# Performance work log

Measured on AMD Instinct MI355X. Metric: run time of the kernel, lower is better.

## Reference

```python
import jax, jax.numpy as jnp
import numpy as np

IMAGE_W = 640
IMAGE_H = 640
ALPHA = 0.25
GAMMA = 2.0
BETA = 1.0 / 9.0
EPS = 1e-4


def _make_anchors(image_w, image_h):
    # standard RetinaNet anchors: 3 ratios x 3 scales per location, 5 FPN levels
    strides = [8, 16, 32, 64, 128]
    base_sizes = [32, 64, 128, 256, 512]
    ratios = np.array([0.5, 1.0, 2.0])
    scales = np.array([2.0 ** 0, 2.0 ** (1.0 / 3.0), 2.0 ** (2.0 / 3.0)])
    all_boxes = []
    for s, b in zip(strides, base_sizes):
        fw, fh = image_w // s, image_h // s
        ws, hs = [], []
        for r in ratios:
            for sc in scales:
                area = (b * sc) ** 2
                w = np.sqrt(area / r)
                ws.append(w)
                hs.append(w * r)
        wh = np.stack([np.array(ws), np.array(hs)], axis=-1).reshape(1, -1, 2)
        cx = (np.arange(fw) + 0.5) * s
        cy = (np.arange(fh) + 0.5) * s
        cx, cy = np.meshgrid(cx, cy)
        ctr = np.stack([cx, cy], axis=-1).reshape(-1, 1, 2)
        boxes = np.concatenate([ctr - 0.5 * wh, ctr + 0.5 * wh], axis=-1).reshape(-1, 4)
        all_boxes.append(boxes)
    return np.concatenate(all_boxes, axis=0).astype(np.float32)  # [76725, 4]


def setup_inputs() -> dict:
    key = jax.random.key(0)
    k1, k2, k3, k4, k5 = jax.random.split(key, 5)
    B, C, M = 4, 80, 16
    anchors = jnp.asarray(_make_anchors(IMAGE_W, IMAGE_H))  # [N,4]
    N = anchors.shape[0]
    batch_anchors = jnp.broadcast_to(anchors[None], (B, N, 4))
    cls_heads = jax.random.uniform(k1, (B, N, C), minval=0.01, maxval=0.99, dtype=jnp.float32)
    reg_heads = jax.random.normal(k2, (B, N, 4), dtype=jnp.float32)
    xy = jax.random.uniform(k3, (B, M, 2), minval=0.0, maxval=480.0)
    wh = jax.random.uniform(k4, (B, M, 2), minval=32.0, maxval=160.0)
    boxes = jnp.concatenate([xy, jnp.minimum(xy + wh, 639.0)], axis=-1)
    labels = jax.random.randint(k5, (B, M), 0, C).astype(jnp.float32)
    valid = jnp.arange(M)[None, :] < 12  # last 4 gt slots are -1 padding
    annotations = jnp.where(valid[..., None],
                            jnp.concatenate([boxes, labels[..., None]], axis=-1),
                            -1.0)
    return {"cls_heads": cls_heads, "reg_heads": reg_heads,
            "batch_anchors": batch_anchors, "annotations": annotations}


def _assign_one_image(anchors, annots):
    # anchors [N,4], annots [M,5] (label<0 == padding)
    valid_gt = annots[:, 4] >= 0.0                                  # [M]
    boxes, cls = annots[:, :4], annots[:, 4]
    area_a = (anchors[:, 2] - anchors[:, 0]) * (anchors[:, 3] - anchors[:, 1])
    area_g = (boxes[:, 2] - boxes[:, 0]) * (boxes[:, 3] - boxes[:, 1])
    lt = jnp.maximum(anchors[:, None, :2], boxes[None, :, :2])      # [N,M,2]
    rb = jnp.minimum(anchors[:, None, 2:], boxes[None, :, 2:])
    wh = jnp.clip(rb - lt, 0.0)
    inter = wh[..., 0] * wh[..., 1]                                 # [N,M]
    iou = inter / (area_a[:, None] + area_g[None, :] - inter)
    iou = jnp.where(valid_gt[None, :], iou, -1.0)                   # ignore padded gts
    idx = jnp.argmax(iou, axis=1)                                   # [N]
    overlap = jnp.max(iou, axis=1)
    gt_box = boxes[idx]                                             # [N,4]
    gt_cls = cls[idx]
    # encode gt box as (tx,ty,tw,th) wrt anchor
    a_wh = anchors[:, 2:] - anchors[:, :2]
    a_ctr = anchors[:, :2] + 0.5 * a_wh
    g_wh = jnp.clip(gt_box[:, 2:] - gt_box[:, :2], 1.0)
    g_ctr = gt_box[:, :2] + 0.5 * g_wh
    targets = jnp.concatenate([(g_ctr - a_ctr) / a_wh, jnp.log(g_wh / a_wh)], axis=1)
    targets = targets / jnp.array([0.1, 0.1, 0.2, 0.2], dtype=targets.dtype)
    label = jnp.full_like(overlap, -1.0)
    label = jnp.where(overlap < 0.4, 0.0, label)
    label = jnp.where(overlap > 0.5, gt_cls + 1.0, label)
    label = jnp.where(jnp.any(valid_gt), label, -1.0)               # no gt -> all ignore
    return targets, label


def reference(cls_heads, reg_heads, batch_anchors, annotations):
    # mask (instead of filter) out-of-border anchors: equivalent to dropping them
    a = batch_anchors
    inside = (a[..., 0] > 0) & (a[..., 1] > 0) & (a[..., 2] < IMAGE_W) & (a[..., 3] < IMAGE_H)
    targets, labels = jax.vmap(_assign_one_image)(batch_anchors, annotations)  # [B,N,4],[B,N]
    labels = jnp.where(inside, labels, -1.0)

    cls_mask = labels >= 0.0          # anchors counted in focal loss
    pos_mask = labels > 0.0           # positive anchors
    pos = jnp.sum(pos_mask, axis=1).astype(cls_heads.dtype)  # [B]

    # focal (cls) loss
    p = jnp.clip(cls_heads, EPS, 1.0 - EPS)                   # [B,N,C]
    num_classes = cls_heads.shape[-1]
    gt_onehot = jax.nn.one_hot(labels.astype(jnp.int32), num_classes + 1,
                               dtype=cls_heads.dtype)[..., 1:]  # [B,N,C]
    is_pos = gt_onehot > 0.5
    alpha_f = jnp.where(is_pos, ALPHA, 1.0 - ALPHA)
    pt = jnp.where(is_pos, p, 1.0 - p)
    focal_w = alpha_f * (1.0 - pt) ** GAMMA
    bce = -gt_onehot * jnp.log(p) - (1.0 - gt_onehot) * jnp.log(1.0 - p)
    fl = focal_w * bce
    cls_per_img = jnp.sum(fl * cls_mask[..., None], axis=(1, 2)) / jnp.maximum(pos, 1.0)

    # smooth-L1 (reg) loss over positive anchors
    x = jnp.abs(reg_heads - targets)
    sl1 = jnp.where(x < BETA, 0.5 * x * x / BETA, x - 0.5 * BETA)
    reg_per_img = jnp.sum(sl1 * pos_mask[..., None], axis=(1, 2)) / jnp.maximum(4.0 * pos, 1.0)

    valid_img = pos > 0.0
    n_valid = jnp.maximum(jnp.sum(valid_img.astype(cls_heads.dtype)), 1.0)
    cls_loss = jnp.sum(jnp.where(valid_img, cls_per_img, 0.0)) / n_valid
    reg_loss = jnp.sum(jnp.where(valid_img, reg_per_img, 0.0)) / n_valid
    return (cls_loss, reg_loss)
```

## Files before the change

### kernel.cpp

```cpp
#include <hip/hip_runtime.h>
#include <cmath>

#define GT_CAP 64

typedef float fvec4 __attribute__((ext_vector_type(4)));

__global__ __launch_bounds__(256) void retina_main(
    const float* __restrict__ cls_heads,
    const float* __restrict__ reg_heads,
    const float* __restrict__ anchors,
    const float* __restrict__ annots,
    float* __restrict__ ws,
    int N, int M, int B)
{
    const int b  = blockIdx.y;
    const int n0 = blockIdx.x << 6;
    const int t  = threadIdx.x;

    __shared__ float s_ann[5 * GT_CAP];
    __shared__ float s_lab[64];
    __shared__ float s_red[12];

    const int mm = (M > GT_CAP) ? GT_CAP : M;
    for (int i = t; i < 5 * mm; i += 256)
        s_ann[i] = annots[(size_t)b * 5 * M + i];
    __syncthreads();

    float reg_acc = 0.0f;
    float pos_cnt = 0.0f;
    float label   = -1.0f;
    if (t < 64) {
        const int n = n0 + t;
        if (n < N) {
            const float4 a = *(const float4*)(anchors + (size_t)n * 4);
            const bool inside = (a.x > 0.0f) && (a.y > 0.0f) &&
                                (a.z < 640.0f) && (a.w < 640.0f);
            if (inside) {
                const float area_a = (a.z - a.x) * (a.w - a.y);
                float best = -3.0e38f;
                int   bi   = 0;
                bool  any  = false;
                for (int m = 0; m < mm; ++m) {
                    const float gx1 = s_ann[m*5+0], gy1 = s_ann[m*5+1];
                    const float gx2 = s_ann[m*5+2], gy2 = s_ann[m*5+3];
                    const float gc  = s_ann[m*5+4];
                    float v = -1.0f;
                    if (gc >= 0.0f) {
                        any = true;
                        const float iw = fmaxf(fminf(a.z, gx2) - fmaxf(a.x, gx1), 0.0f);
                        const float ih = fmaxf(fminf(a.w, gy2) - fmaxf(a.y, gy1), 0.0f);
                        const float inter = iw * ih;
                        v = inter / (area_a + (gx2 - gx1) * (gy2 - gy1) - inter);
                    }
                    if (v > best) { best = v; bi = m; }
                }
                if (any) {
                    if (best < 0.4f)      label = 0.0f;
                    else if (best > 0.5f) label = s_ann[bi*5+4] + 1.0f;
                }
                if (label > 0.0f) {
                    pos_cnt = 1.0f;
                    const float aw = a.z - a.x, ah = a.w - a.y;
                    const float acx = a.x + 0.5f * aw, acy = a.y + 0.5f * ah;
                    const float gw = fmaxf(s_ann[bi*5+2] - s_ann[bi*5+0], 1.0f);
                    const float gh = fmaxf(s_ann[bi*5+3] - s_ann[bi*5+1], 1.0f);
                    const float gcx = s_ann[bi*5+0] + 0.5f * gw;
                    const float gcy = s_ann[bi*5+1] + 0.5f * gh;
                    const float tx = (gcx - acx) / aw * 10.0f;
                    const float ty = (gcy - acy) / ah * 10.0f;
                    const float tw = __logf(gw / aw) * 5.0f;
                    const float th = __logf(gh / ah) * 5.0f;
                    const float4 r = *(const float4*)(reg_heads + ((size_t)b * N + n) * 4);
                    const float dx[4] = { fabsf(r.x - tx), fabsf(r.y - ty),
                                          fabsf(r.z - tw), fabsf(r.w - th) };
                    #pragma unroll
                    for (int j = 0; j < 4; ++j) {
                        const float x = dx[j];
                        reg_acc += (x < (1.0f / 9.0f)) ? 4.5f * x * x
                                                       : x - (1.0f / 18.0f);
                    }
                }
            }
        }
        s_lab[t] = label;
    }
    const int anyValid = __syncthreads_or((t < 64 && label >= 0.0f) ? 1 : 0);

    float cls_acc = 0.0f;
    if (anyValid) {
        const float* cls_base = cls_heads + ((size_t)b * N + n0) * 80;
        float labb[5];
        fvec4 pb[5];
        #pragma unroll
        for (int k = 0; k < 5; ++k) {
            const int e = t + (k << 8);
            const int a = e / 20;
            const float lab = s_lab[a];
            fvec4 v = {0.5f, 0.5f, 0.5f, 0.5f};
            if (lab >= 0.0f)
                v = *(const fvec4*)(cls_base + 4 * e);
            labb[k] = lab; pb[k] = v;
        }
        #pragma unroll
        for (int k = 0; k < 5; ++k) {
            const int e  = t + (k << 8);
            const int c4 = e - (e / 20) * 20;
            const float lab  = labb[k];
            const fvec4 v    = pb[k];
            const float mask = (lab >= 0.0f) ? 1.0f : 0.0f;
            const float pv[4] = { v.x, v.y, v.z, v.w };
            const float cb = (float)(c4 * 4 + 1);
            float local = 0.0f;
            #pragma unroll
            for (int j = 0; j < 4; ++j) {
                const float p = fminf(fmaxf(pv[j], 1.0e-4f), 1.0f - 1.0e-4f);
                const bool  is_pos = (lab == cb + (float)j);
                const float pt     = is_pos ? p : 1.0f - p;
                const float alpha  = is_pos ? 0.25f : 0.75f;
                const float om     = 1.0f - pt;
                local += alpha * om * om * (-__logf(pt));
            }
            cls_acc += mask * local;
        }
    }

    const int lane = t & 63, wid = t >> 6;
    #pragma unroll
    for (int off = 32; off > 0; off >>= 1) {
        cls_acc += __shfl_down(cls_acc, off, 64);
        reg_acc += __shfl_down(reg_acc, off, 64);
        pos_cnt += __shfl_down(pos_cnt, off, 64);
    }
    if (lane == 0) {
        s_red[wid]     = cls_acc;
        s_red[4 + wid] = reg_acc;
        s_red[8 + wid] = pos_cnt;
    }
    __syncthreads();
    if (t == 0) {
        const float c = s_red[0] + s_red[1] + s_red[2]  + s_red[3];
        const float r = s_red[4] + s_red[5] + s_red[6]  + s_red[7];
        const float p = s_red[8] + s_red[9] + s_red[10] + s_red[11];
        if (c != 0.0f) atomicAdd(&ws[b], c);
        if (r != 0.0f) atomicAdd(&ws[B + b], r);
        if (p != 0.0f) atomicAdd(&ws[2 * B + b], p);
    }
}

__global__ void retina_final(const float* __restrict__ ws,
                             float* __restrict__ out, int B)
{
    if (threadIdx.x == 0 && blockIdx.x == 0) {
        float cl = 0.0f, rl = 0.0f, nv = 0.0f;
        for (int b = 0; b < B; ++b) {
            const float pos = ws[2 * B + b];
            if (pos > 0.0f) {
                cl += ws[b]     / fmaxf(pos, 1.0f);
                rl += ws[B + b] / fmaxf(4.0f * pos, 1.0f);
                nv += 1.0f;
            }
        }
        const float n = fmaxf(nv, 1.0f);
        out[0] = cl / n;
        out[1] = rl / n;
    }
}

extern "C" void kernel_launch(void* const* d_in, const int* in_sizes, int n_in,
                              void* d_out, int out_size, void* d_ws, size_t ws_size,
                              hipStream_t stream) {
    const float* cls = (const float*)d_in[0];
    const float* reg = (const float*)d_in[1];
    const float* anc = (const float*)d_in[2];
    const float* ann = (const float*)d_in[3];

    const int B = 4;
    const int N = in_sizes[1] / (4 * B);
    const int M = in_sizes[3] / (5 * B);
    float* ws = (float*)d_ws;

    (void)hipMemsetAsync(d_ws, 0, 12 * sizeof(float), stream);

    dim3 grid((N + 63) / 64, B);
    retina_main<<<grid, 256, 0, stream>>>(cls, reg, anc, ann, ws, N, M, B);
    retina_final<<<1, 64, 0, stream>>>(ws, (float*)d_out, B);
}
```

Measured before the change: 199.2 us.

## Prefetch class tile into LDS asynchronously while computing anchor assignment

Each block now covers 128 anchors, up from 64, and issues global_load_lds async copies of the whole 128x80 class tile into shared memory before the IoU assignment runs. The cls load thus overlaps the anchor/GT matching instead of starting after the label barrier. The annotation staging in shared memory is dropped in favor of direct global reads. The change always loads cls data, even for ignored anchors, and uses about 40KB of LDS per block, which may reduce occupancy. Bandwidth is also wasted on tiles whose anchors are all outside the image.

Result: faster. 175.7 us (-11.8%).

```diff
diff --git a/kernel.cpp b/kernel.cpp
--- a/kernel.cpp
+++ b/kernel.cpp
@@ -1,9 +1,15 @@
 #include <hip/hip_runtime.h>
 #include <cmath>
 
-#define GT_CAP 64
 
 typedef float fvec4 __attribute__((ext_vector_type(4)));
+
+__device__ __forceinline__ void async_ld16(const float* g, float* l) {
+    __builtin_amdgcn_global_load_lds(
+        (const __attribute__((address_space(1))) unsigned int*)g,
+        (__attribute__((address_space(3))) unsigned int*)l,
+        16, 0, 0);
+}
 
 __global__ __launch_bounds__(256) void retina_main(
     const float* __restrict__ cls_heads,
@@ -14,36 +20,42 @@
     int N, int M, int B)
 {
     const int b  = blockIdx.y;
-    const int n0 = blockIdx.x << 6;
+    const int n0 = blockIdx.x << 7;
     const int t  = threadIdx.x;
 
-    __shared__ float s_ann[5 * GT_CAP];
-    __shared__ float s_lab[64];
+    __shared__ float s_cls[128 * 80];
+    __shared__ float s_lab[128];
     __shared__ float s_red[12];
 
-    const int mm = (M > GT_CAP) ? GT_CAP : M;
-    for (int i = t; i < 5 * mm; i += 256)
-        s_ann[i] = annots[(size_t)b * 5 * M + i];
-    __syncthreads();
+    const int tile   = (N - n0 < 128) ? (N - n0) : 128;
+    const int valid4 = tile * 20;
+    const float* gbase = cls_heads + ((size_t)b * N + n0) * 80;
+    #pragma unroll
+    for (int k = 0; k < 10; ++k) {
+        const int idx  = (k << 8) + t;
+        const int gidx = (idx < valid4) ? idx : 0;
+        async_ld16(gbase + 4 * gidx, &s_cls[4 * idx]);
+    }
 
     float reg_acc = 0.0f;
     float pos_cnt = 0.0f;
     float label   = -1.0f;
-    if (t < 64) {
+    if (t < 128) {
         const int n = n0 + t;
         if (n < N) {
             const float4 a = *(const float4*)(anchors + (size_t)n * 4);
             const bool inside = (a.x > 0.0f) && (a.y > 0.0f) &&
                                 (a.z < 640.0f) && (a.w < 640.0f);
             if (inside) {
+                const float* ann = annots + (size_t)b * 5 * M;
                 const float area_a = (a.z - a.x) * (a.w - a.y);
                 float best = -3.0e38f;
                 int   bi   = 0;
                 bool  any  = false;
-                for (int m = 0; m < mm; ++m) {
-                    const float gx1 = s_ann[m*5+0], gy1 = s_ann[m*5+1];
-                    const float gx2 = s_ann[m*5+2], gy2 = s_ann[m*5+3];
-                    const float gc  = s_ann[m*5+4];
+                for (int m = 0; m < M; ++m) {
+                    const float gx1 = ann[m*5+0], gy1 = ann[m*5+1];
+                    const float gx2 = ann[m*5+2], gy2 = ann[m*5+3];
+                    const float gc  = ann[m*5+4];
                     float v = -1.0f;
                     if (gc >= 0.0f) {
                         any = true;
@@ -56,16 +68,16 @@
                 }
                 if (any) {
                     if (best < 0.4f)      label = 0.0f;
-                    else if (best > 0.5f) label = s_ann[bi*5+4] + 1.0f;
+                    else if (best > 0.5f) label = ann[bi*5+4] + 1.0f;
                 }
                 if (label > 0.0f) {
                     pos_cnt = 1.0f;
                     const float aw = a.z - a.x, ah = a.w - a.y;
                     const float acx = a.x + 0.5f * aw, acy = a.y + 0.5f * ah;
-                    const float gw = fmaxf(s_ann[bi*5+2] - s_ann[bi*5+0], 1.0f);
-                    const float gh = fmaxf(s_ann[bi*5+3] - s_ann[bi*5+1], 1.0f);
-                    const float gcx = s_ann[bi*5+0] + 0.5f * gw;
-                    const float gcy = s_ann[bi*5+1] + 0.5f * gh;
+                    const float gw = fmaxf(ann[bi*5+2] - ann[bi*5+0], 1.0f);
+                    const float gh = fmaxf(ann[bi*5+3] - ann[bi*5+1], 1.0f);
+                    const float gcx = ann[bi*5+0] + 0.5f * gw;
+                    const float gcy = ann[bi*5+1] + 0.5f * gh;
                     const float tx = (gcx - acx) / aw * 10.0f;
                     const float ty = (gcy - acy) / ah * 10.0f;
                     const float tw = __logf(gw / aw) * 5.0f;
@@ -84,43 +96,34 @@
         }
         s_lab[t] = label;
     }
-    const int anyValid = __syncthreads_or((t < 64 && label >= 0.0f) ? 1 : 0);
+
+    __builtin_amdgcn_s_waitcnt(0);
+    const int anyValid = __syncthreads_or(label >= 0.0f ? 1 : 0);
 
     float cls_acc = 0.0f;
     if (anyValid) {
-        const float* cls_base = cls_heads + ((size_t)b * N + n0) * 80;
-        float labb[5];
-        fvec4 pb[5];
         #pragma unroll
-        for (int k = 0; k < 5; ++k) {
-            const int e = t + (k << 8);
-            const int a = e / 20;
+        for (int k = 0; k < 10; ++k) {
+            const int e  = (k << 8) + t;
+            const int a  = e / 20;
+            const int c4 = e - a * 20;
             const float lab = s_lab[a];
-            fvec4 v = {0.5f, 0.5f, 0.5f, 0.5f};
-            if (lab >= 0.0f)
-                v = *(const fvec4*)(cls_base + 4 * e);
-            labb[k] = lab; pb[k] = v;
-        }
-        #pragma unroll
-        for (int k = 0; k < 5; ++k) {
-            const int e  = t + (k << 8);
-            const int c4 = e - (e / 20) * 20;
-            const float lab  = labb[k];
-            const fvec4 v    = pb[k];
-            const float mask = (lab >= 0.0f) ? 1.0f : 0.0f;
-            const float pv[4] = { v.x, v.y, v.z, v.w };
-            const float cb = (float)(c4 * 4 + 1);
-            float local = 0.0f;
-            #pragma unroll
-            for (int j = 0; j < 4; ++j) {
-                const float p = fminf(fmaxf(pv[j], 1.0e-4f), 1.0f - 1.0e-4f);
-                const bool  is_pos = (lab == cb + (float)j);
-                const float pt     = is_pos ? p : 1.0f - p;
-                const float alpha  = is_pos ? 0.25f : 0.75f;
-                const float om     = 1.0f - pt;
-                local += alpha * om * om * (-__logf(pt));
+            if (lab >= 0.0f) {
+                const fvec4 v = *(const fvec4*)&s_cls[4 * e];
+                const float pv[4] = { v.x, v.y, v.z, v.w };
+                const float cb = (float)(c4 * 4 + 1);
+                float local = 0.0f;
+                #pragma unroll
+                for (int j = 0; j < 4; ++j) {
+                    const float p = fminf(fmaxf(pv[j], 1.0e-4f), 1.0f - 1.0e-4f);
+                    const bool  is_pos = (lab == cb + (float)j);
+                    const float pt     = is_pos ? p : 1.0f - p;
+                    const float alpha  = is_pos ? 0.25f : 0.75f;
+                    const float om     = 1.0f - pt;
+                    local += alpha * om * om * (-__logf(pt));
+                }
+                cls_acc += local;
             }
-            cls_acc += mask * local;
         }
     }
 
@@ -181,7 +184,7 @@
 
     (void)hipMemsetAsync(d_ws, 0, 12 * sizeof(float), stream);
 
-    dim3 grid((N + 63) / 64, B);
+    dim3 grid((N + 127) / 128, B);
     retina_main<<<grid, 256, 0, stream>>>(cls, reg, anc, ann, ws, N, M, B);
     retina_final<<<1, 64, 0, stream>>>(ws, (float*)d_out, B);
 }
```

## Split anchor assignment and focal loss into separate kernels

Applied to the files above, without the earlier changes.

Anchor assignment moves into its own kernel that uses all 256 threads per block, one anchor each, and writes per-anchor labels to workspace memory. A separate focal-loss kernel then streams the class scores, eight vec4 loads per thread, reading those labels back. This removes the old design where only 64 of 256 threads did the IoU assignment while the rest waited. In exchange it adds a kernel launch and a global round trip for the labels, and it drops both the skip of class loads for ignored anchors and the GT_CAP bound on M.

Result: faster. 177.8 us (-10.8%).

```diff
diff --git a/kernel.cpp b/kernel.cpp
--- a/kernel.cpp
+++ b/kernel.cpp
@@ -1,149 +1,162 @@
 #include <hip/hip_runtime.h>
 #include <cmath>
 
-#define GT_CAP 64
 
 typedef float fvec4 __attribute__((ext_vector_type(4)));
 
-__global__ __launch_bounds__(256) void retina_main(
-    const float* __restrict__ cls_heads,
+__global__ __launch_bounds__(256) void retina_assign(
     const float* __restrict__ reg_heads,
     const float* __restrict__ anchors,
     const float* __restrict__ annots,
     float* __restrict__ ws,
+    float* __restrict__ labf,
     int N, int M, int B)
 {
-    const int b  = blockIdx.y;
-    const int n0 = blockIdx.x << 6;
-    const int t  = threadIdx.x;
-
-    __shared__ float s_ann[5 * GT_CAP];
-    __shared__ float s_lab[64];
-    __shared__ float s_red[12];
-
-    const int mm = (M > GT_CAP) ? GT_CAP : M;
-    for (int i = t; i < 5 * mm; i += 256)
+    const int b = blockIdx.y;
+    const int t = threadIdx.x;
+    const int n = (blockIdx.x << 8) + t;
+
+    __shared__ float s_ann[5 * 64];
+    __shared__ float s_red[8];
+
+    for (int i = t; i < 5 * M; i += 256)
         s_ann[i] = annots[(size_t)b * 5 * M + i];
     __syncthreads();
 
     float reg_acc = 0.0f;
     float pos_cnt = 0.0f;
     float label   = -1.0f;
-    if (t < 64) {
-        const int n = n0 + t;
-        if (n < N) {
-            const float4 a = *(const float4*)(anchors + (size_t)n * 4);
-            const bool inside = (a.x > 0.0f) && (a.y > 0.0f) &&
-                                (a.z < 640.0f) && (a.w < 640.0f);
-            if (inside) {
-                const float area_a = (a.z - a.x) * (a.w - a.y);
-                float best = -3.0e38f;
-                int   bi   = 0;
-                bool  any  = false;
-                for (int m = 0; m < mm; ++m) {
-                    const float gx1 = s_ann[m*5+0], gy1 = s_ann[m*5+1];
-                    const float gx2 = s_ann[m*5+2], gy2 = s_ann[m*5+3];
-                    const float gc  = s_ann[m*5+4];
-                    float v = -1.0f;
-                    if (gc >= 0.0f) {
-                        any = true;
-                        const float iw = fmaxf(fminf(a.z, gx2) - fmaxf(a.x, gx1), 0.0f);
-                        const float ih = fmaxf(fminf(a.w, gy2) - fmaxf(a.y, gy1), 0.0f);
-                        const float inter = iw * ih;
-                        v = inter / (area_a + (gx2 - gx1) * (gy2 - gy1) - inter);
-                    }
-                    if (v > best) { best = v; bi = m; }
+    if (n < N) {
+        const float4 a = *(const float4*)(anchors + (size_t)n * 4);
+        const bool inside = (a.x > 0.0f) && (a.y > 0.0f) &&
+                            (a.z < 640.0f) && (a.w < 640.0f);
+        if (inside) {
+            const float area_a = (a.z - a.x) * (a.w - a.y);
+            float best = -3.0e38f;
+            int   bi   = 0;
+            bool  any  = false;
+            for (int m = 0; m < M; ++m) {
+                const float gx1 = s_ann[m*5+0], gy1 = s_ann[m*5+1];
+                const float gx2 = s_ann[m*5+2], gy2 = s_ann[m*5+3];
+                const float gc  = s_ann[m*5+4];
+                float v = -1.0f;
+                if (gc >= 0.0f) {
+                    any = true;
+                    const float iw = fmaxf(fminf(a.z, gx2) - fmaxf(a.x, gx1), 0.0f);
+                    const float ih = fmaxf(fminf(a.w, gy2) - fmaxf(a.y, gy1), 0.0f);
+                    const float inter = iw * ih;
+                    v = inter / (area_a + (gx2 - gx1) * (gy2 - gy1) - inter);
                 }
-                if (any) {
-                    if (best < 0.4f)      label = 0.0f;
-                    else if (best > 0.5f) label = s_ann[bi*5+4] + 1.0f;
+                if (v > best) { best = v; bi = m; }
+            }
+            if (any) {
+                if (best < 0.4f)      label = 0.0f;
+                else if (best > 0.5f) label = s_ann[bi*5+4] + 1.0f;
+            }
+            if (label > 0.0f) {
+                pos_cnt = 1.0f;
+                const float aw = a.z - a.x, ah = a.w - a.y;
+                const float acx = a.x + 0.5f * aw, acy = a.y + 0.5f * ah;
+                const float gw = fmaxf(s_ann[bi*5+2] - s_ann[bi*5+0], 1.0f);
+                const float gh = fmaxf(s_ann[bi*5+3] - s_ann[bi*5+1], 1.0f);
+                const float gcx = s_ann[bi*5+0] + 0.5f * gw;
+                const float gcy = s_ann[bi*5+1] + 0.5f * gh;
+                const float tx = (gcx - acx) / aw * 10.0f;
+                const float ty = (gcy - acy) / ah * 10.0f;
+                const float tw = __logf(gw / aw) * 5.0f;
+                const float th = __logf(gh / ah) * 5.0f;
+                const float4 r = *(const float4*)(reg_heads + ((size_t)b * N + n) * 4);
+                const float dx[4] = { fabsf(r.x - tx), fabsf(r.y - ty),
+                                      fabsf(r.z - tw), fabsf(r.w - th) };
+                #pragma unroll
+                for (int j = 0; j < 4; ++j) {
+                    const float x = dx[j];
+                    reg_acc += (x < (1.0f / 9.0f)) ? 4.5f * x * x
+                                                   : x - (1.0f / 18.0f);
                 }
-                if (label > 0.0f) {
-                    pos_cnt = 1.0f;
-                    const float aw = a.z - a.x, ah = a.w - a.y;
-                    const float acx = a.x + 0.5f * aw, acy = a.y + 0.5f * ah;
-                    const float gw = fmaxf(s_ann[bi*5+2] - s_ann[bi*5+0], 1.0f);
-                    const float gh = fmaxf(s_ann[bi*5+3] - s_ann[bi*5+1], 1.0f);
-                    const float gcx = s_ann[bi*5+0] + 0.5f * gw;
-                    const float gcy = s_ann[bi*5+1] + 0.5f * gh;
-                    const float tx = (gcx - acx) / aw * 10.0f;
-                    const float ty = (gcy - acy) / ah * 10.0f;
-                    const float tw = __logf(gw / aw) * 5.0f;
-                    const float th = __logf(gh / ah) * 5.0f;
-                    const float4 r = *(const float4*)(reg_heads + ((size_t)b * N + n) * 4);
-                    const float dx[4] = { fabsf(r.x - tx), fabsf(r.y - ty),
-                                          fabsf(r.z - tw), fabsf(r.w - th) };
-                    #pragma unroll
-                    for (int j = 0; j < 4; ++j) {
-                        const float x = dx[j];
-                        reg_acc += (x < (1.0f / 9.0f)) ? 4.5f * x * x
-                                                       : x - (1.0f / 18.0f);
-                    }
-                }
             }
         }
-        s_lab[t] = label;
-    }
-    const int anyValid = __syncthreads_or((t < 64 && label >= 0.0f) ? 1 : 0);
-
-    float cls_acc = 0.0f;
-    if (anyValid) {
-        const float* cls_base = cls_heads + ((size_t)b * N + n0) * 80;
-        float labb[5];
-        fvec4 pb[5];
-        #pragma unroll
-        for (int k = 0; k < 5; ++k) {
-            const int e = t + (k << 8);
-            const int a = e / 20;
-            const float lab = s_lab[a];
-            fvec4 v = {0.5f, 0.5f, 0.5f, 0.5f};
-            if (lab >= 0.0f)
-                v = *(const fvec4*)(cls_base + 4 * e);
-            labb[k] = lab; pb[k] = v;
-        }
-        #pragma unroll
-        for (int k = 0; k < 5; ++k) {
-            const int e  = t + (k << 8);
-            const int c4 = e - (e / 20) * 20;
-            const float lab  = labb[k];
-            const fvec4 v    = pb[k];
-            const float mask = (lab >= 0.0f) ? 1.0f : 0.0f;
-            const float pv[4] = { v.x, v.y, v.z, v.w };
-            const float cb = (float)(c4 * 4 + 1);
-            float local = 0.0f;
-            #pragma unroll
-            for (int j = 0; j < 4; ++j) {
-                const float p = fminf(fmaxf(pv[j], 1.0e-4f), 1.0f - 1.0e-4f);
-                const bool  is_pos = (lab == cb + (float)j);
-                const float pt     = is_pos ? p : 1.0f - p;
-                const float alpha  = is_pos ? 0.25f : 0.75f;
-                const float om     = 1.0f - pt;
-                local += alpha * om * om * (-__logf(pt));
-            }
-            cls_acc += mask * local;
-        }
+        labf[(size_t)b * N + n] = label;
     }
 
     const int lane = t & 63, wid = t >> 6;
     #pragma unroll
     for (int off = 32; off > 0; off >>= 1) {
-        cls_acc += __shfl_down(cls_acc, off, 64);
         reg_acc += __shfl_down(reg_acc, off, 64);
         pos_cnt += __shfl_down(pos_cnt, off, 64);
     }
-    if (lane == 0) {
-        s_red[wid]     = cls_acc;
-        s_red[4 + wid] = reg_acc;
-        s_red[8 + wid] = pos_cnt;
-    }
+    if (lane == 0) { s_red[wid] = reg_acc; s_red[4 + wid] = pos_cnt; }
     __syncthreads();
     if (t == 0) {
-        const float c = s_red[0] + s_red[1] + s_red[2]  + s_red[3];
-        const float r = s_red[4] + s_red[5] + s_red[6]  + s_red[7];
-        const float p = s_red[8] + s_red[9] + s_red[10] + s_red[11];
+        const float r = s_red[0] + s_red[1] + s_red[2] + s_red[3];
+        const float p = s_red[4] + s_red[5] + s_red[6] + s_red[7];
+        if (r != 0.0f) atomicAdd(&ws[4 + b], r);
+        if (p != 0.0f) atomicAdd(&ws[8 + b], p);
+    }
+}
+
+__global__ __launch_bounds__(256, 4) void retina_focal(
+    const float* __restrict__ cls_heads,
+    const float* __restrict__ labf,
+    float* __restrict__ ws,
+    int N, int B)
+{
+    const int b = blockIdx.y;
+    const int t = threadIdx.x;
+    const int E = N * 20;
+    const int base = (blockIdx.x << 11) + t;
+
+    const float* lab_b = labf + (size_t)b * N;
+    const fvec4* cls_b = (const fvec4*)(cls_heads + (size_t)b * N * 80);
+
+    int   ec[8]; float inr[8];
+    #pragma unroll
+    for (int k = 0; k < 8; ++k) {
+        const int e = base + (k << 8);
+        const int ok = (e < E);
+        inr[k] = ok ? 1.0f : 0.0f;
+        ec[k]  = ok ? e : 0;
+    }
+    int a[8], c4[8];
+    #pragma unroll
+    for (int k = 0; k < 8; ++k) { a[k] = ec[k] / 20; c4[k] = ec[k] - 20 * a[k]; }
+
+    float lab[8];
+    #pragma unroll
+    for (int k = 0; k < 8; ++k) lab[k] = lab_b[a[k]];
+    fvec4 p4[8];
+    #pragma unroll
+    for (int k = 0; k < 8; ++k) p4[k] = cls_b[ec[k]];
+
+    float cls_acc = 0.0f;
+    #pragma unroll
+    for (int k = 0; k < 8; ++k) {
+        const float mask = (lab[k] >= 0.0f) ? inr[k] : 0.0f;
+        const float pv[4] = { p4[k].x, p4[k].y, p4[k].z, p4[k].w };
+        const float cb = (float)(c4[k] * 4 + 1);
+        float local = 0.0f;
+        #pragma unroll
+        for (int j = 0; j < 4; ++j) {
+            const float p = fminf(fmaxf(pv[j], 1.0e-4f), 1.0f - 1.0e-4f);
+            const bool  is_pos = (lab[k] == cb + (float)j);
+            const float pt     = is_pos ? p : 1.0f - p;
+            const float alpha  = is_pos ? 0.25f : 0.75f;
+            const float om     = 1.0f - pt;
+            local += alpha * om * om * (-__logf(pt));
+        }
+        cls_acc += mask * local;
+    }
+
+    __shared__ float s_red[4];
+    const int lane = t & 63, wid = t >> 6;
+    #pragma unroll
+    for (int off = 32; off > 0; off >>= 1)
+        cls_acc += __shfl_down(cls_acc, off, 64);
+    if (lane == 0) s_red[wid] = cls_acc;
+    __syncthreads();
+    if (t == 0) {
+        const float c = s_red[0] + s_red[1] + s_red[2] + s_red[3];
         if (c != 0.0f) atomicAdd(&ws[b], c);
-        if (r != 0.0f) atomicAdd(&ws[B + b], r);
-        if (p != 0.0f) atomicAdd(&ws[2 * B + b], p);
     }
 }
 
@@ -153,10 +166,10 @@
     if (threadIdx.x == 0 && blockIdx.x == 0) {
         float cl = 0.0f, rl = 0.0f, nv = 0.0f;
         for (int b = 0; b < B; ++b) {
-            const float pos = ws[2 * B + b];
+            const float pos = ws[8 + b];
             if (pos > 0.0f) {
                 cl += ws[b]     / fmaxf(pos, 1.0f);
-                rl += ws[B + b] / fmaxf(4.0f * pos, 1.0f);
+                rl += ws[4 + b] / fmaxf(4.0f * pos, 1.0f);
                 nv += 1.0f;
             }
         }
@@ -177,11 +190,17 @@
     const int B = 4;
     const int N = in_sizes[1] / (4 * B);
     const int M = in_sizes[3] / (5 * B);
-    float* ws = (float*)d_ws;
+    float* ws   = (float*)d_ws;
+    float* labf = ws + 16;
 
     (void)hipMemsetAsync(d_ws, 0, 12 * sizeof(float), stream);
 
-    dim3 grid((N + 63) / 64, B);
-    retina_main<<<grid, 256, 0, stream>>>(cls, reg, anc, ann, ws, N, M, B);
+    dim3 gridA((N + 255) / 256, B);
+    retina_assign<<<gridA, 256, 0, stream>>>(reg, anc, ann, ws, labf, N, M, B);
+
+    const int E = N * 20;
+    dim3 gridB((E + 2047) / 2048, B);
+    retina_focal<<<gridB, 256, 0, stream>>>(cls, labf, ws, N, B);
+
     retina_final<<<1, 64, 0, stream>>>(ws, (float*)d_out, B);
 }
```
